# Kernel tuning notes

Hardware: AMD Instinct MI355X
Metric: run time of the kernel (lower is better)

Reference implementation:

```python
import jax, jax.numpy as jnp
import numpy as np

B, S, HID = 4, 2048, 2048
NH, NKV, D = 16, 8, 128
RK, RV = 16, 16
HPG = NH // NKV
SCALING = D ** -0.5
NEG = -1e9


def _rope(x, cos, sin):
    # x: [B, S, H, D]; cos/sin: [S, D//2]. Gemma split-half complex rotation.
    x1, x2 = jnp.split(x, 2, axis=-1)
    c = cos[None, :, None, :]
    s = sin[None, :, None, :]
    return jnp.concatenate([x1 * c - x2 * s, x1 * s + x2 * c], axis=-1)


def setup_inputs() -> dict:
    key = jax.random.key(0)
    ks = jax.random.split(key, 8)
    hidden_states = jax.random.normal(ks[0], (B, S, HID), dtype=jnp.float32)
    # RoPE frequencies (theta=10000)
    inv_freq = 1.0 / (10000.0 ** (np.arange(0, D, 2, dtype=np.float32) / D))
    ang = np.arange(S, dtype=np.float32)[:, None] * inv_freq[None, :]
    freqs_cos = jnp.asarray(np.cos(ang), dtype=jnp.float32)
    freqs_sin = jnp.asarray(np.sin(ang), dtype=jnp.float32)
    kv_write_indices = jnp.arange(S, dtype=jnp.int32)
    # causal additive mask [1,1,S,S]
    causal = jnp.tril(jnp.ones((S, S), dtype=bool))
    mask = jnp.where(causal, 0.0, NEG).astype(jnp.float32)[None, None]
    sc = 0.02
    W_q = jax.random.normal(ks[1], (NH * D, HID), dtype=jnp.float32) * sc
    W_k = jax.random.normal(ks[2], (NKV * D, HID), dtype=jnp.float32) * sc
    W_v = jax.random.normal(ks[3], (NKV * D, HID), dtype=jnp.float32) * sc
    o_proj_w = jax.random.normal(ks[4], (HID, NH * D), dtype=jnp.float32) * sc
    V_r_basis = jax.random.normal(ks[5], (NH, D, RK), dtype=jnp.float32) * (D ** -0.5)
    Z_v_basis = jax.random.normal(ks[6], (NKV, D, RV), dtype=jnp.float32) * (D ** -0.5)
    return {"hidden_states": hidden_states, "freqs_cos": freqs_cos, "freqs_sin": freqs_sin,
            "kv_write_indices": kv_write_indices, "mask": mask, "W_q": W_q, "W_k": W_k,
            "W_v": W_v, "o_proj_w": o_proj_w, "V_r_basis": V_r_basis, "Z_v_basis": Z_v_basis}


def reference(hidden_states, freqs_cos, freqs_sin, kv_write_indices, mask,
              W_q, W_k, W_v, o_proj_w, V_r_basis, Z_v_basis):
    bsz, q_len, _ = hidden_states.shape
    q = (hidden_states @ W_q.T).reshape(bsz, q_len, NH, D)
    k = (hidden_states @ W_k.T).reshape(bsz, q_len, NKV, D)
    v = (hidden_states @ W_v.T).reshape(bsz, q_len, NKV, D)

    # project K per-head onto its group's basis (vectorized over the head loop)
    head_to_group = jnp.arange(NH) // HPG                       # [NH]
    k_per_head = k[:, :, head_to_group, :]                      # [B,S,NH,D]
    pk = jnp.einsum('bshd,hdr->bshr', k_per_head, V_r_basis)    # [B,S,NH,RK]
    pv = jnp.einsum('bqgd,gdr->bqgr', v, Z_v_basis)             # [B,S,NKV,RV]

    # factorized cache write (scatter along seq dim), prefill: kv_seq_len = S
    kv_seq_len = q_len
    cache_pk = jnp.zeros((bsz, kv_seq_len, NH, RK), hidden_states.dtype)
    cache_pv = jnp.zeros((bsz, kv_seq_len, NKV, RV), hidden_states.dtype)
    cache_pk = cache_pk.at[:, kv_write_indices].set(pk)
    cache_pv = cache_pv.at[:, kv_write_indices].set(pv)

    # reconstruct K/V from compressed cache
    k_hat = jnp.einsum('bshr,hrd->bshd', cache_pk, jnp.swapaxes(V_r_basis, -1, -2))
    v_hat = jnp.einsum('bsgr,grd->bsgd', cache_pv, jnp.swapaxes(Z_v_basis, -1, -2))

    # RoPE post-reconstruction
    q_rot = _rope(q, freqs_cos[:q_len], freqs_sin[:q_len])
    k_rot = _rope(k_hat, freqs_cos[:kv_seq_len], freqs_sin[:kv_seq_len])

    # GQA: repeat kv heads
    v_g = jnp.repeat(v_hat, HPG, axis=2)                        # [B,S,NH,D]

    scores = jnp.einsum('bqhd,bkhd->bhqk', q_rot, k_rot) * SCALING
    scores = scores + mask[:, :, :q_len, :kv_seq_len]
    probs = jax.nn.softmax(scores.astype(jnp.float32), axis=-1).astype(hidden_states.dtype)
    out = jnp.einsum('bhqk,bkhd->bqhd', probs, v_g)
    out = out.reshape(bsz, q_len, NH * D)
    return out @ o_proj_w.T
```

## Files before the change

### kernel.cpp

```cpp
#include <hip/hip_runtime.h>

typedef unsigned short ushort8 __attribute__((ext_vector_type(8)));
typedef short s16x8 __attribute__((ext_vector_type(8)));
typedef float f32x4 __attribute__((ext_vector_type(4)));

#define AS1 __attribute__((address_space(1)))
#define AS3 __attribute__((address_space(3)))

#define B_    4
#define S_    2048
#define HID_  2048
#define NH_   16
#define NKV_  8
#define D_    128
#define RK_   16
#define SCALING_ 0.08838834764831845f
#define LOG2E_   1.4426950408889634f
#define NEGBIG   -1.0e30f

__device__ __forceinline__ float bf2f(unsigned short u) {
  union { unsigned int i; float f; } x; x.i = ((unsigned int)u) << 16; return x.f;
}
__device__ __forceinline__ unsigned short f2bf(float f) {
  union { float f; unsigned int i; } x; x.f = f;
  unsigned int r = x.i + 0x7fffu + ((x.i >> 16) & 1u);
  return (unsigned short)(r >> 16);
}

__global__ __launch_bounds__(256) void cvt_bf16(const float* __restrict__ in,
                                                unsigned short* __restrict__ out,
                                                int n8) {
  int i = blockIdx.x * 256 + threadIdx.x;
  const int stride = gridDim.x * 256;
  for (; i < n8; i += stride) {
    const float4 a = ((const float4*)in)[i * 2];
    const float4 b = ((const float4*)in)[i * 2 + 1];
    ushort8 u;
    u[0] = f2bf(a.x); u[1] = f2bf(a.y); u[2] = f2bf(a.z); u[3] = f2bf(a.w);
    u[4] = f2bf(b.x); u[5] = f2bf(b.y); u[6] = f2bf(b.z); u[7] = f2bf(b.w);
    *(ushort8*)&out[i * 8] = u;
  }
}

__global__ __launch_bounds__(256) void wfuse(const float* __restrict__ W_k,
                                             const float* __restrict__ W_v,
                                             const float* __restrict__ Vr,
                                             const float* __restrict__ Zv,
                                             unsigned short* __restrict__ Wf) {
  const int idx = blockIdx.x;
  const int cc = blockIdx.y * 256;
  const int tid = threadIdx.x;
  const bool isK = idx < 16;
  const int hg = isK ? idx : (idx - 16);
  const int wrow0 = isK ? (idx * 16) : (256 + (idx - 16) * 16);
  const float* W = isK ? &W_k[(size_t)((hg >> 1) * 128) * HID_]
                       : &W_v[(size_t)(hg * 128) * HID_];
  const float* P = isK ? &Vr[(size_t)hg * 128 * 16] : &Zv[(size_t)hg * 128 * 16];
  __shared__ float Wl[32][257];
  float acc[16] = {};
  for (int d0 = 0; d0 < 128; d0 += 32) {
    __syncthreads();
#pragma unroll 8
    for (int dd = 0; dd < 32; ++dd)
      Wl[dd][tid] = W[(size_t)(d0 + dd) * HID_ + cc + tid];
    __syncthreads();
#pragma unroll 8
    for (int dd = 0; dd < 32; ++dd) {
      const float w = Wl[dd][tid];
#pragma unroll
      for (int r = 0; r < 16; ++r) acc[r] += w * P[(d0 + dd) * 16 + r];
    }
  }
#pragma unroll
  for (int r = 0; r < 16; ++r)
    Wf[(size_t)(wrow0 + r) * HID_ + cc + tid] = f2bf(acc[r]);
}

template<bool CBF>
__global__ __launch_bounds__(256) void gemm_mfma(const unsigned short* __restrict__ A,
                                                 const unsigned short* __restrict__ Bb,
                                                 void* __restrict__ C_,
                                                 int M, int N, int K) {
  __shared__ unsigned short Ash[128 * 64];
  __shared__ unsigned short Bsh[128 * 64];
  const int tid = threadIdx.x;
  const int w = tid >> 6, l = tid & 63, lg = l >> 4, ll = l & 15;
  const int wr = w >> 1, wc = w & 1;
  const int flat = blockIdx.y * gridDim.x + blockIdx.x;
  const int cpx = (gridDim.x * gridDim.y) >> 3;
  const int swz = (flat & 7) * cpx + (flat >> 3);
  const int bm = (swz / gridDim.x) * 128, bn = (swz % gridDim.x) * 128;

  f32x4 acc[4][4];
#pragma unroll
  for (int i = 0; i < 4; i++)
#pragma unroll
    for (int j = 0; j < 4; j++) acc[i][j] = (f32x4){0.f, 0.f, 0.f, 0.f};

  const int srow = tid >> 3;
  const int sslot = tid & 7;

  for (int k0 = 0; k0 < K; k0 += 64) {
    __syncthreads();
#pragma unroll
    for (int c = 0; c < 4; ++c) {
      const int row = c * 32 + srow;
      const int ss = sslot ^ (row & 7);
      const unsigned short* srcA = &A[(size_t)(bm + row) * K + k0 + ss * 8];
      const unsigned short* srcB = &Bb[(size_t)(bn + row) * K + k0 + ss * 8];
      char* dstA = ((char*)Ash) + c * 4096 + w * 1024;
      char* dstB = ((char*)Bsh) + c * 4096 + w * 1024;
      __builtin_amdgcn_global_load_lds((const AS1 void*)srcA, (AS3 void*)dstA, 16, 0, 0);
      __builtin_amdgcn_global_load_lds((const AS1 void*)srcB, (AS3 void*)dstB, 16, 0, 0);
    }
    __syncthreads();

#pragma unroll
    for (int ks = 0; ks < 2; ++ks) {
      s16x8 af[4], bf_[4];
#pragma unroll
      for (int mi = 0; mi < 4; ++mi) {
        const int row = wr * 64 + mi * 16 + ll;
        af[mi] = *(const s16x8*)&Ash[row * 64 + (((ks * 4 + lg) ^ (row & 7)) * 8)];
      }
#pragma unroll
      for (int ni = 0; ni < 4; ++ni) {
        const int row = wc * 64 + ni * 16 + ll;
        bf_[ni] = *(const s16x8*)&Bsh[row * 64 + (((ks * 4 + lg) ^ (row & 7)) * 8)];
      }
#pragma unroll
      for (int mi = 0; mi < 4; ++mi)
#pragma unroll
        for (int ni = 0; ni < 4; ++ni)
          acc[mi][ni] = __builtin_amdgcn_mfma_f32_16x16x32_bf16(af[mi], bf_[ni], acc[mi][ni], 0, 0, 0);
    }
  }

#pragma unroll
  for (int mi = 0; mi < 4; ++mi)
#pragma unroll
    for (int ni = 0; ni < 4; ++ni)
#pragma unroll
      for (int j = 0; j < 4; ++j) {
        const int row = bm + wr * 64 + mi * 16 + lg * 4 + j;
        const int col = bn + wc * 64 + ni * 16 + ll;
        if (CBF) ((unsigned short*)C_)[(size_t)row * N + col] = f2bf(acc[mi][ni][j]);
        else     ((float*)C_)[(size_t)row * N + col] = acc[mi][ni][j];
      }
}

template<bool CBF>
__global__ __launch_bounds__(512) void gemm256_8ph(const unsigned short* __restrict__ A,
                                                   const unsigned short* __restrict__ Bb,
                                                   void* __restrict__ C_,
                                                   int M, int N, int K) {
  __shared__ unsigned short Lds[2][2][256 * 64];
  const int tid = threadIdx.x;
  const int w = tid >> 6, l = tid & 63, lg = l >> 4, ll = l & 15;
  const int wr = w >> 2;
  const int wc = w & 3;
  const int flat = blockIdx.y * gridDim.x + blockIdx.x;
  const int cpx = (gridDim.x * gridDim.y) >> 3;
  const int swz = (flat & 7) * cpx + (flat >> 3);
  const int bm = (swz / gridDim.x) * 256, bn = (swz % gridDim.x) * 256;

  f32x4 acc[8][4];
#pragma unroll
  for (int i = 0; i < 8; i++)
#pragma unroll
    for (int j = 0; j < 4; j++) acc[i][j] = (f32x4){0.f, 0.f, 0.f, 0.f};

  auto stage = [&](int op, int hh, int slot, int kk) {
    const unsigned short* base = (op == 0) ? A : Bb;
    const int r0 = (op == 0) ? bm : bn;
#pragma unroll
    for (int i = 0; i < 2; ++i) {
      const int r = hh * 128 + i * 64 + (tid >> 3);
      const int ss = (tid & 7) ^ (r & 7);
      const unsigned short* src = &base[(size_t)(r0 + r) * K + kk + ss * 8];
      unsigned short* dstb = &Lds[slot][op][(hh * 128 + i * 64 + (w << 3)) * 64];
      __builtin_amdgcn_global_load_lds((const AS1 void*)src, (AS3 void*)dstb, 16, 0, 0);
    }
  };

  const int NT = K >> 6;

  stage(0, 0, 0, 0);
  stage(1, 0, 0, 0);
  stage(1, 1, 0, 0);
  stage(0, 1, 0, 0);

#define GPHASE(MIH, NIH, WAITN, DO_PF)                                          \
  {                                                                             \
    if (WAITN == 4)      asm volatile("s_waitcnt vmcnt(4)" ::: "memory");       \
    else if (WAITN == 6) asm volatile("s_waitcnt vmcnt(6)" ::: "memory");       \
    __builtin_amdgcn_sched_barrier(0);                                          \
    __builtin_amdgcn_s_barrier();                                               \
    __builtin_amdgcn_sched_barrier(0);                                          \
    s16x8 af[4][2], bf_[2][2];                                                  \
    _Pragma("unroll")                                                           \
    for (int mi2 = 0; mi2 < 4; ++mi2)                                           \
      _Pragma("unroll")                                                         \
      for (int ks = 0; ks < 2; ++ks) {                                          \
        const int row = (MIH) * 128 + wr * 64 + mi2 * 16 + ll;                  \
        af[mi2][ks] = *(const s16x8*)&Lds[s][0][row * 64 +                      \
                          (((ks * 4 + lg) ^ (row & 7)) * 8)];                   \
      }                                                                         \
    _Pragma("unroll")                                                           \
    for (int ni2 = 0; ni2 < 2; ++ni2)                                           \
      _Pragma("unroll")                                                         \
      for (int ks = 0; ks < 2; ++ks) {                                          \
        const int row = (NIH) * 128 + wc * 32 + ni2 * 16 + ll;                  \
        bf_[ni2][ks] = *(const s16x8*)&Lds[s][1][row * 64 +                     \
                          (((ks * 4 + lg) ^ (row & 7)) * 8)];                   \
      }                                                                         \
    __builtin_amdgcn_s_setprio(1);                                              \
    _Pragma("unroll")                                                           \
    for (int mi2 = 0; mi2 < 4; ++mi2)                                           \
      _Pragma("unroll")                                                         \
      for (int ni2 = 0; ni2 < 2; ++ni2)                                         \
        _Pragma("unroll")                                                       \
        for (int ks = 0; ks < 2; ++ks)                                          \
          acc[(MIH) * 4 + mi2][(NIH) * 2 + ni2] =                               \
              __builtin_amdgcn_mfma_f32_16x16x32_bf16(                          \
                  af[mi2][ks], bf_[ni2][ks],                                    \
                  acc[(MIH) * 4 + mi2][(NIH) * 2 + ni2], 0, 0, 0);              \
    __builtin_amdgcn_s_setprio(0);                                              \
    DO_PF                                                                       \
  }

  for (int t = 0; t < NT; ++t) {
    const int s = t & 1;
    const int s2 = s ^ 1;
    const bool hn = (t + 1 < NT);
    const int k1 = (t + 1) << 6;
    GPHASE(0, 0, 4, { if (hn) { stage(0, 0, s2, k1); stage(1, 0, s2, k1); } })
    GPHASE(0, 1, 6, { if (hn) { stage(1, 1, s2, k1); } })
    GPHASE(1, 1, 6, { if (hn) { stage(0, 1, s2, k1); } })
    GPHASE(1, 0, 0, {})
  }
#undef GPHASE

#pragma unroll
  for (int mih = 0; mih < 2; ++mih)
#pragma unroll
    for (int mi2 = 0; mi2 < 4; ++mi2)
#pragma unroll
      for (int nih = 0; nih < 2; ++nih)
#pragma unroll
        for (int ni2 = 0; ni2 < 2; ++ni2)
#pragma unroll
          for (int j = 0; j < 4; ++j) {
            const int row = bm + mih * 128 + wr * 64 + mi2 * 16 + lg * 4 + j;
            const int col = bn + nih * 128 + wc * 32 + ni2 * 16 + ll;
            const float v = acc[mih * 4 + mi2][nih * 2 + ni2][j];
            if (CBF) ((unsigned short*)C_)[(size_t)row * N + col] = f2bf(v);
            else     ((float*)C_)[(size_t)row * N + col] = v;
          }
}

__global__ __launch_bounds__(256) void rope_q(unsigned short* __restrict__ q,
                                              const float* __restrict__ cosT,
                                              const float* __restrict__ sinT) {
  const int p = blockIdx.x * 256 + threadIdx.x;
  const int d = p & 63;
  const int h = (p >> 6) & 15;
  const int s = (p >> 10) & 2047;
  const int b = p >> 21;
  const size_t base = (((size_t)b * S_ + s) * NH_ + h) * D_ + d;
  const float x1 = bf2f(q[base]), x2 = bf2f(q[base + 64]);
  const float c = cosT[s * 64 + d], sn = sinT[s * 64 + d];
  const float sc = SCALING_ * LOG2E_;
  q[base]      = f2bf((x1 * c - x2 * sn) * sc);
  q[base + 64] = f2bf((x1 * sn + x2 * c) * sc);
}

__global__ __launch_bounds__(256) void expand_k(const float* __restrict__ pkpv,
                                                const float* __restrict__ Vr,
                                                const float* __restrict__ cosT,
                                                const float* __restrict__ sinT,
                                                unsigned short* __restrict__ kr) {
  const int s0 = blockIdx.x * 32, h = blockIdx.y, b = blockIdx.z;
  const int tid = threadIdx.x;
  __shared__ float pkS[32][17];
  if (tid < 128) {
    const int r_ = tid >> 2, c4 = (tid & 3) * 4;
    float4 v = *(const float4*)&pkpv[(size_t)(b * S_ + s0 + r_) * 384 + h * 16 + c4];
    pkS[r_][c4 + 0] = v.x; pkS[r_][c4 + 1] = v.y;
    pkS[r_][c4 + 2] = v.z; pkS[r_][c4 + 3] = v.w;
  }
  __syncthreads();
  const int row = tid >> 3, dl = tid & 7;
  float kh[16];
#pragma unroll
  for (int j = 0; j < 16; j++) {
    const int d = dl + 8 * j;
    const float4* w = (const float4*)&Vr[((size_t)h * D_ + d) * RK_];
    float a = 0.f;
#pragma unroll
    for (int q4 = 0; q4 < 4; q4++) {
      float4 wv = w[q4];
      a += pkS[row][q4 * 4 + 0] * wv.x + pkS[row][q4 * 4 + 1] * wv.y
         + pkS[row][q4 * 4 + 2] * wv.z + pkS[row][q4 * 4 + 3] * wv.w;
    }
    kh[j] = a;
  }
  const int pos = s0 + row;
  const size_t o = (((size_t)b * NH_ + h) * S_ + pos) * D_;
#pragma unroll
  for (int j = 0; j < 8; j++) {
    const int d = dl + 8 * j;
    const float c = cosT[pos * 64 + d], sn = sinT[pos * 64 + d];
    kr[o + d]      = f2bf(kh[j] * c - kh[j + 8] * sn);
    kr[o + d + 64] = f2bf(kh[j] * sn + kh[j + 8] * c);
  }
}

__global__ __launch_bounds__(256) void expand_v(const float* __restrict__ pkpv,
                                                const float* __restrict__ Zv,
                                                unsigned short* __restrict__ vh) {
  const int s0 = blockIdx.x * 32, g = blockIdx.y, b = blockIdx.z;
  const int tid = threadIdx.x;
  __shared__ float pvS[32][17];
  if (tid < 128) {
    const int r_ = tid >> 2, c4 = (tid & 3) * 4;
    float4 v = *(const float4*)&pkpv[(size_t)(b * S_ + s0 + r_) * 384 + 256 + g * 16 + c4];
    pvS[r_][c4 + 0] = v.x; pvS[r_][c4 + 1] = v.y;
    pvS[r_][c4 + 2] = v.z; pvS[r_][c4 + 3] = v.w;
  }
  __syncthreads();
  const int row = tid >> 3, dl = tid & 7;
  const size_t o = (((size_t)b * NKV_ + g) * S_ + s0 + row) * D_;
#pragma unroll
  for (int j = 0; j < 16; j++) {
    const int d = dl + 8 * j;
    const float4* w = (const float4*)&Zv[((size_t)g * D_ + d) * RK_];
    float a = 0.f;
#pragma unroll
    for (int q4 = 0; q4 < 4; q4++) {
      float4 wv = w[q4];
      a += pvS[row][q4 * 4 + 0] * wv.x + pvS[row][q4 * 4 + 1] * wv.y
         + pvS[row][q4 * 4 + 2] * wv.z + pvS[row][q4 * 4 + 3] * wv.w;
    }
    vh[o + d] = f2bf(a);
  }
}

template<bool SPLIT>
__global__ __launch_bounds__(256) void attn_mfma(const unsigned short* __restrict__ q,
                                                 const unsigned short* __restrict__ kr,
                                                 const unsigned short* __restrict__ vh,
                                                 unsigned short* __restrict__ outp,
                                                 unsigned short* __restrict__ P0,
                                                 unsigned short* __restrict__ P1,
                                                 float2* __restrict__ ml0,
                                                 float2* __restrict__ ml1) {
  int qt, h, b, half;
  if constexpr (SPLIT) {
    const int flat = ((int)blockIdx.z * 16 + (int)blockIdx.y) * 32 + (int)blockIdx.x;
    const int swz = (flat & 7) * 256 + (flat >> 3);
    qt = 15 - (swz & 15);
    half = (swz >> 4) & 1;
    h = (swz >> 5) & 15;
    b = swz >> 9;
  } else {
    const int flat = ((int)blockIdx.z * 16 + (int)blockIdx.y) * 16 + (int)blockIdx.x;
    const int swz = (flat & 7) * 128 + (flat >> 3);
    qt = 15 - (swz & 15);
    half = 0;
    h = (swz >> 4) & 15;
    b = swz >> 8;
  }
  const int g = h >> 1;
  const int tid = threadIdx.x;
  const int w = tid >> 6, l = tid & 63, lg = l >> 4, ll = l & 15;

  __shared__ unsigned short Klds[2][64 * 128];
  __shared__ unsigned short Vt[2][128 * 64];
  __shared__ unsigned short Ps[4][32 * 64];

  const int qr0 = qt * 128 + w * 32;
  const int kt0   = SPLIT ? (half ? qt + 1 : 0)          : 0;
  const int ktend = SPLIT ? (half ? 2 * qt + 1 : qt)     : 2 * qt + 1;
  const int kmy = 2 * qt + (w >> 1);

  s16x8 qf[2][4];
#pragma unroll
  for (int mi = 0; mi < 2; ++mi)
#pragma unroll
    for (int ks = 0; ks < 4; ++ks)
      qf[mi][ks] = *(const s16x8*)&q[(((size_t)b * S_ + qr0 + mi * 16 + ll) * NH_ + h) * D_ + ks * 32 + lg * 8];

  f32x4 o[2][8];
#pragma unroll
  for (int mi = 0; mi < 2; ++mi)
#pragma unroll
    for (int nd = 0; nd < 8; ++nd) o[mi][nd] = (f32x4){0.f, 0.f, 0.f, 0.f};
  float m_[2][4], l_[2][4];
#pragma unroll
  for (int mi = 0; mi < 2; ++mi)
#pragma unroll
    for (int j = 0; j < 4; ++j) { m_[mi][j] = NEGBIG; l_[mi][j] = 0.f; }

  const unsigned short* kbase = &kr[(((size_t)b * NH_ + h) * S_) * D_];
  const unsigned short* vbase = &vh[(((size_t)b * NKV_ + g) * S_) * D_];
  const int vk = (tid & 31) * 2, d0v = (tid >> 5) * 16;

  ushort8 va0, va1, vb0, vb1;
  {
    const unsigned short* kb0 = kbase + (size_t)kt0 * 64 * D_;
#pragma unroll
    for (int c = 0; c < 4; ++c) {
      const int ro = c * 16 + w * 4 + lg;
      const int ss = ll ^ (ro & 7);
      const unsigned short* src = kb0 + ro * D_ + ss * 8;
      char* dst = ((char*)&Klds[0][0]) + c * 4096 + w * 1024;
      __builtin_amdgcn_global_load_lds((const AS1 void*)src, (AS3 void*)dst, 16, 0, 0);
    }
    const unsigned short* v0 = vbase + (size_t)(kt0 * 64 + vk) * D_ + d0v;
    va0 = *(const ushort8*)v0; va1 = *(const ushort8*)(v0 + 8);
    vb0 = *(const ushort8*)(v0 + D_); vb1 = *(const ushort8*)(v0 + D_ + 8);
#pragma unroll
    for (int j = 0; j < 8; ++j) {
      const int d1 = d0v + j, d2 = d0v + 8 + j;
      *(unsigned int*)&Vt[0][d1 * 64 + (((vk >> 3) ^ (d1 & 7)) * 8) + (vk & 7)] =
          (unsigned int)va0[j] | ((unsigned int)vb0[j] << 16);
      *(unsigned int*)&Vt[0][d2 * 64 + (((vk >> 3) ^ (d2 & 7)) * 8) + (vk & 7)] =
          (unsigned int)va1[j] | ((unsigned int)vb1[j] << 16);
    }
  }
  __syncthreads();

  for (int kt = kt0; kt <= ktend; ++kt) {
    const int p = (kt - kt0) & 1;
    if (kt < ktend) {
      const unsigned short* kb2 = kbase + (size_t)(kt + 1) * 64 * D_;
#pragma unroll
      for (int c = 0; c < 4; ++c) {
        const int ro = c * 16 + w * 4 + lg;
        const int ss = ll ^ (ro & 7);
        const unsigned short* src = kb2 + ro * D_ + ss * 8;
        char* dst = ((char*)&Klds[p ^ 1][0]) + c * 4096 + w * 1024;
        __builtin_amdgcn_global_load_lds((const AS1 void*)src, (AS3 void*)dst, 16, 0, 0);
      }
      const unsigned short* v0 = vbase + (size_t)((kt + 1) * 64 + vk) * D_ + d0v;
      va0 = *(const ushort8*)v0; va1 = *(const ushort8*)(v0 + 8);
      vb0 = *(const ushort8*)(v0 + D_); vb1 = *(const ushort8*)(v0 + D_ + 8);
    }

    if (kt <= kmy) {
      f32x4 s[2][4];
#pragma unroll
      for (int mi = 0; mi < 2; ++mi)
#pragma unroll
        for (int ni = 0; ni < 4; ++ni) s[mi][ni] = (f32x4){0.f, 0.f, 0.f, 0.f};
#pragma unroll
      for (int ks = 0; ks < 4; ++ks) {
#pragma unroll
        for (int ni = 0; ni < 4; ++ni) {
          const int row = ni * 16 + ll;
          const s16x8 kf = *(const s16x8*)&Klds[p][row * 128 + (((ks * 4 + lg) ^ (row & 7)) * 8)];
          s[0][ni] = __builtin_amdgcn_mfma_f32_16x16x32_bf16(qf[0][ks], kf, s[0][ni], 0, 0, 0);
          s[1][ni] = __builtin_amdgcn_mfma_f32_16x16x32_bf16(qf[1][ks], kf, s[1][ni], 0, 0, 0);
        }
      }

      const bool diag = (kt == kmy);
      float lm[2][4];
#pragma unroll
      for (int mi = 0; mi < 2; ++mi)
#pragma unroll
        for (int j = 0; j < 4; ++j) {
          if (diag) {
            const int qg = qr0 + mi * 16 + lg * 4 + j;
#pragma unroll
            for (int ni = 0; ni < 4; ++ni)
              if (kt * 64 + ni * 16 + ll > qg) s[mi][ni][j] = NEGBIG;
          }
          lm[mi][j] = fmaxf(fmaxf(s[mi][0][j], s[mi][1][j]),
                            fmaxf(s[mi][2][j], s[mi][3][j]));
        }
      float excess = lm[0][0] - m_[0][0];
#pragma unroll
      for (int mi = 0; mi < 2; ++mi)
#pragma unroll
        for (int j = 0; j < 4; ++j) excess = fmaxf(excess, lm[mi][j] - m_[mi][j]);
      const bool slow = __any(excess > 11.5f);

#pragma unroll
      for (int mi = 0; mi < 2; ++mi)
#pragma unroll
        for (int j = 0; j < 4; ++j) {
          float ps_[4];
          if (slow) {
            float mt = lm[mi][j];
            mt = fmaxf(mt, __shfl_xor(mt, 1));
            mt = fmaxf(mt, __shfl_xor(mt, 2));
            mt = fmaxf(mt, __shfl_xor(mt, 4));
            mt = fmaxf(mt, __shfl_xor(mt, 8));
            const float mnew = fmaxf(m_[mi][j], mt);
            const float al = exp2f(m_[mi][j] - mnew);
            m_[mi][j] = mnew;
            float sum = 0.f;
#pragma unroll
            for (int ni = 0; ni < 4; ++ni) { ps_[ni] = exp2f(s[mi][ni][j] - mnew); sum += ps_[ni]; }
            l_[mi][j] = l_[mi][j] * al + sum;
#pragma unroll
            for (int nd = 0; nd < 8; ++nd) o[mi][nd][j] *= al;
          } else {
            float sum = 0.f;
#pragma unroll
            for (int ni = 0; ni < 4; ++ni) { ps_[ni] = exp2f(s[mi][ni][j] - m_[mi][j]); sum += ps_[ni]; }
            l_[mi][j] += sum;
          }
          const int prow = mi * 16 + lg * 4 + j;
#pragma unroll
          for (int nq = 0; nq < 2; ++nq) {
            unsigned int u;
            asm("v_cvt_pk_bf16_f32 %0, %1, %2" : "=v"(u) : "v"(ps_[nq * 2]), "v"(ps_[nq * 2 + 1]));
            const int c0 = nq * 32 + ll, c1 = nq * 32 + 16 + ll;
            Ps[w][prow * 64 + (((c0 >> 3) ^ (prow & 7)) * 8) + (ll & 7)] = (unsigned short)u;
            Ps[w][prow * 64 + (((c1 >> 3) ^ (prow & 7)) * 8) + (ll & 7)] = (unsigned short)(u >> 16);
          }
        }

      s16x8 pa[2][2];
#pragma unroll
      for (int mi = 0; mi < 2; ++mi)
#pragma unroll
        for (int ks2 = 0; ks2 < 2; ++ks2) {
          const int prow = mi * 16 + ll;
          pa[mi][ks2] = *(const s16x8*)&Ps[w][prow * 64 + (((ks2 * 4 + lg) ^ (prow & 7)) * 8)];
        }
#pragma unroll
      for (int nd = 0; nd < 8; ++nd) {
#pragma unroll
        for (int ks2 = 0; ks2 < 2; ++ks2) {
          const int vr = nd * 16 + ll;
          const s16x8 vbf = *(const s16x8*)&Vt[p][vr * 64 + (((ks2 * 4 + lg) ^ (vr & 7)) * 8)];
          o[0][nd] = __builtin_amdgcn_mfma_f32_16x16x32_bf16(pa[0][ks2], vbf, o[0][nd], 0, 0, 0);
          o[1][nd] = __builtin_amdgcn_mfma_f32_16x16x32_bf16(pa[1][ks2], vbf, o[1][nd], 0, 0, 0);
        }
      }
    }

    if (kt < ktend) {
#pragma unroll
      for (int j = 0; j < 8; ++j) {
        const int d1 = d0v + j, d2 = d0v + 8 + j;
        *(unsigned int*)&Vt[p ^ 1][d1 * 64 + (((vk >> 3) ^ (d1 & 7)) * 8) + (vk & 7)] =
            (unsigned int)va0[j] | ((unsigned int)vb0[j] << 16);
        *(unsigned int*)&Vt[p ^ 1][d2 * 64 + (((vk >> 3) ^ (d2 & 7)) * 8) + (vk & 7)] =
            (unsigned int)va1[j] | ((unsigned int)vb1[j] << 16);
      }
    }
    __syncthreads();
  }

#pragma unroll
  for (int mi = 0; mi < 2; ++mi)
#pragma unroll
    for (int j = 0; j < 4; ++j) {
      float ls = l_[mi][j];
      ls += __shfl_xor(ls, 1);
      ls += __shfl_xor(ls, 2);
      ls += __shfl_xor(ls, 4);
      ls += __shfl_xor(ls, 8);
      if constexpr (SPLIT) {
        unsigned short* Ph = half ? P1 : P0;
        float2* mlh = half ? ml1 : ml0;
        const size_t ridx = ((size_t)b * NH_ + h) * S_ + qr0 + mi * 16 + lg * 4 + j;
        unsigned short* op = &Ph[ridx * D_ + ll];
#pragma unroll
        for (int nd = 0; nd < 8; ++nd) op[nd * 16] = f2bf(o[mi][nd][j]);
        if (ll == 0) mlh[ridx] = make_float2(m_[mi][j], ls);
      } else {
        const float inv = 1.f / ls;
        const size_t rowg = (size_t)b * S_ + qr0 + mi * 16 + lg * 4 + j;
        unsigned short* op = &outp[rowg * (NH_ * D_) + h * D_ + ll];
#pragma unroll
        for (int nd = 0; nd < 8; ++nd) op[nd * 16] = f2bf(o[mi][nd][j] * inv);
      }
    }
}

__global__ __launch_bounds__(256) void attn_combine(const unsigned short* __restrict__ P0,
                                                    const unsigned short* __restrict__ P1,
                                                    const float2* __restrict__ ml0,
                                                    const float2* __restrict__ ml1,
                                                    unsigned short* __restrict__ outp) {
  const int s = blockIdx.x, b = blockIdx.y;
  const int tid = threadIdx.x;
  const int h = tid >> 4, d0 = (tid & 15) * 8;
  const size_t ridx = ((size_t)b * NH_ + h) * S_ + s;
  const float2 a = ml0[ridx], c = ml1[ridx];
  const float m = fmaxf(a.x, c.x);
  const float a0 = exp2f(a.x - m), a1 = exp2f(c.x - m);
  const float inv = 1.f / (a0 * a.y + a1 * c.y);
  const ushort8 u0 = *(const ushort8*)&P0[ridx * D_ + d0];
  const ushort8 u1 = *(const ushort8*)&P1[ridx * D_ + d0];
  ushort8 r;
#pragma unroll
  for (int j = 0; j < 8; ++j)
    r[j] = f2bf((a0 * bf2f(u0[j]) + a1 * bf2f(u1[j])) * inv);
  *(ushort8*)&outp[((size_t)b * S_ + s) * (NH_ * D_) + h * D_ + d0] = r;
}

extern "C" void kernel_launch(void* const* d_in, const int* in_sizes, int n_in,
                              void* d_out, int out_size, void* d_ws, size_t ws_size,
                              hipStream_t stream) {
  const float* hidden = (const float*)d_in[0];
  const float* cosT   = (const float*)d_in[1];
  const float* sinT   = (const float*)d_in[2];
  const float* W_q    = (const float*)d_in[5];
  const float* W_k    = (const float*)d_in[6];
  const float* W_v    = (const float*)d_in[7];
  const float* W_o    = (const float*)d_in[8];
  const float* Vr     = (const float*)d_in[9];
  const float* Zv     = (const float*)d_in[10];
  float* out = (float*)d_out;

  char* ws = (char*)d_ws;
  unsigned short* hb     = (unsigned short*)(ws + 0);
  unsigned short* attn_b = (unsigned short*)(ws + 0);
  unsigned short* P0     = (unsigned short*)(ws + 0);
  unsigned short* q_b    = (unsigned short*)(ws + 33554432);
  unsigned short* kr_b   = (unsigned short*)(ws + 67108864);
  unsigned short* Wf     = (unsigned short*)(ws + 100663296);
  unsigned short* vh_b   = (unsigned short*)(ws + 100663296);
  unsigned short* WR1    = (unsigned short*)(ws + 117440512);
  float*          pkpv   = (float*)(ws + 117440512);
  unsigned short* P1     = (unsigned short*)(ws + 130023424);
  float2*         ml0    = (float2*)(ws + 163577856);
  float2*         ml1    = (float2*)(ws + 164626432);
  const size_t NEED_SPLIT = 165675008ull;
  const bool split = (ws_size >= NEED_SPLIT);

  const int M = B_ * S_;

  cvt_bf16<<<2048, 256, 0, stream>>>(hidden, hb, (B_ * S_ * HID_) / 8);
  cvt_bf16<<<2048, 256, 0, stream>>>(W_q, WR1, (HID_ * HID_) / 8);
  gemm256_8ph<true><<<dim3(8, 32), 512, 0, stream>>>(hb, WR1, q_b, M, 2048, HID_);

  wfuse<<<dim3(24, 8), 256, 0, stream>>>(W_k, W_v, Vr, Zv, Wf);
  gemm_mfma<false><<<dim3(3, 64), 256, 0, stream>>>(hb, Wf, pkpv, M, 384, HID_);

  rope_q<<<(B_ * S_ * NH_ * 64) / 256, 256, 0, stream>>>(q_b, cosT, sinT);

  expand_k<<<dim3(S_ / 32, NH_, B_), 256, 0, stream>>>(pkpv, Vr, cosT, sinT, kr_b);
  expand_v<<<dim3(S_ / 32, NKV_, B_), 256, 0, stream>>>(pkpv, Zv, vh_b);

  cvt_bf16<<<2048, 256, 0, stream>>>(W_o, WR1, (HID_ * HID_) / 8);

  if (split) {
    attn_mfma<true><<<dim3(32, 16, 4), 256, 0, stream>>>(q_b, kr_b, vh_b, nullptr,
                                                         P0, P1, ml0, ml1);
    attn_combine<<<dim3(S_, B_), 256, 0, stream>>>(P0, P1, ml0, ml1, q_b);
    gemm256_8ph<false><<<dim3(8, 32), 512, 0, stream>>>(q_b, WR1, out, M, HID_, HID_);
  } else {
    attn_mfma<false><<<dim3(16, 16, 4), 256, 0, stream>>>(q_b, kr_b, vh_b, attn_b,
                                                          nullptr, nullptr, nullptr, nullptr);
    gemm256_8ph<false><<<dim3(8, 32), 512, 0, stream>>>(attn_b, WR1, out, M, HID_, HID_);
  }
}
```

Baseline: 708.0 us.

## Split attention query tile across eight waves of sixteen rows each

The attention kernel moves from 4 waves of 32 query rows to 8 waves of 16 query rows per 128-row tile, at 512 threads per block. K/V tile loads are spread over twice as many threads, and per-wave register state (Q fragments, accumulators, softmax stats) is halved. The aim is more waves to hide latency and lower register pressure. The cost is that each K/V fragment read from LDS now feeds one MFMA instead of two, which doubles LDS read traffic per FLOP, and the larger blocks add barrier cost.

```diff
diff --git a/kernel.cpp b/kernel.cpp
--- a/kernel.cpp
+++ b/kernel.cpp
@@ -347,7 +347,7 @@
 }
 
 template<bool SPLIT>
-__global__ __launch_bounds__(256) void attn_mfma(const unsigned short* __restrict__ q,
+__global__ __launch_bounds__(512) void attn_mfma(const unsigned short* __restrict__ q,
                                                  const unsigned short* __restrict__ kr,
                                                  const unsigned short* __restrict__ vh,
                                                  unsigned short* __restrict__ outp,
@@ -377,56 +377,48 @@
 
   __shared__ unsigned short Klds[2][64 * 128];
   __shared__ unsigned short Vt[2][128 * 64];
-  __shared__ unsigned short Ps[4][32 * 64];
-
-  const int qr0 = qt * 128 + w * 32;
-  const int kt0   = SPLIT ? (half ? qt + 1 : 0)          : 0;
-  const int ktend = SPLIT ? (half ? 2 * qt + 1 : qt)     : 2 * qt + 1;
-  const int kmy = 2 * qt + (w >> 1);
-
-  s16x8 qf[2][4];
-#pragma unroll
-  for (int mi = 0; mi < 2; ++mi)
-#pragma unroll
-    for (int ks = 0; ks < 4; ++ks)
-      qf[mi][ks] = *(const s16x8*)&q[(((size_t)b * S_ + qr0 + mi * 16 + ll) * NH_ + h) * D_ + ks * 32 + lg * 8];
-
-  f32x4 o[2][8];
-#pragma unroll
-  for (int mi = 0; mi < 2; ++mi)
-#pragma unroll
-    for (int nd = 0; nd < 8; ++nd) o[mi][nd] = (f32x4){0.f, 0.f, 0.f, 0.f};
-  float m_[2][4], l_[2][4];
-#pragma unroll
-  for (int mi = 0; mi < 2; ++mi)
-#pragma unroll
-    for (int j = 0; j < 4; ++j) { m_[mi][j] = NEGBIG; l_[mi][j] = 0.f; }
+  __shared__ unsigned short Ps[8][16 * 64];
+
+  const int qr0 = qt * 128 + w * 16;
+  const int kt0   = SPLIT ? (half ? qt + 1 : 0)      : 0;
+  const int ktend = SPLIT ? (half ? 2 * qt + 1 : qt) : 2 * qt + 1;
+  const int kmy = 2 * qt + (w >> 2);
+
+  s16x8 qf[4];
+#pragma unroll
+  for (int ks = 0; ks < 4; ++ks)
+    qf[ks] = *(const s16x8*)&q[(((size_t)b * S_ + qr0 + ll) * NH_ + h) * D_ + ks * 32 + lg * 8];
+
+  f32x4 o[8];
+#pragma unroll
+  for (int nd = 0; nd < 8; ++nd) o[nd] = (f32x4){0.f, 0.f, 0.f, 0.f};
+  float m_[4], l_[4];
+#pragma unroll
+  for (int j = 0; j < 4; ++j) { m_[j] = NEGBIG; l_[j] = 0.f; }
 
   const unsigned short* kbase = &kr[(((size_t)b * NH_ + h) * S_) * D_];
   const unsigned short* vbase = &vh[(((size_t)b * NKV_ + g) * S_) * D_];
-  const int vk = (tid & 31) * 2, d0v = (tid >> 5) * 16;
-
-  ushort8 va0, va1, vb0, vb1;
+  const int vk = (tid & 31) * 2;
+  const int vd0 = (tid >> 5) * 8;
+
+  ushort8 va, vb2;
   {
     const unsigned short* kb0 = kbase + (size_t)kt0 * 64 * D_;
 #pragma unroll
-    for (int c = 0; c < 4; ++c) {
-      const int ro = c * 16 + w * 4 + lg;
-      const int ss = ll ^ (ro & 7);
-      const unsigned short* src = kb0 + ro * D_ + ss * 8;
-      char* dst = ((char*)&Klds[0][0]) + c * 4096 + w * 1024;
+    for (int c = 0; c < 2; ++c) {
+      const int row = c * 32 + (tid >> 4);
+      const int ss = (tid & 15) ^ (row & 7);
+      const unsigned short* src = kb0 + row * D_ + ss * 8;
+      char* dst = ((char*)&Klds[0][0]) + c * 8192 + w * 1024;
       __builtin_amdgcn_global_load_lds((const AS1 void*)src, (AS3 void*)dst, 16, 0, 0);
     }
-    const unsigned short* v0 = vbase + (size_t)(kt0 * 64 + vk) * D_ + d0v;
-    va0 = *(const ushort8*)v0; va1 = *(const ushort8*)(v0 + 8);
-    vb0 = *(const ushort8*)(v0 + D_); vb1 = *(const ushort8*)(v0 + D_ + 8);
+    const unsigned short* v0 = vbase + (size_t)(kt0 * 64 + vk) * D_ + vd0;
+    va = *(const ushort8*)v0; vb2 = *(const ushort8*)(v0 + D_);
 #pragma unroll
     for (int j = 0; j < 8; ++j) {
-      const int d1 = d0v + j, d2 = d0v + 8 + j;
-      *(unsigned int*)&Vt[0][d1 * 64 + (((vk >> 3) ^ (d1 & 7)) * 8) + (vk & 7)] =
-          (unsigned int)va0[j] | ((unsigned int)vb0[j] << 16);
-      *(unsigned int*)&Vt[0][d2 * 64 + (((vk >> 3) ^ (d2 & 7)) * 8) + (vk & 7)] =
-          (unsigned int)va1[j] | ((unsigned int)vb1[j] << 16);
+      const int d = vd0 + j;
+      *(unsigned int*)&Vt[0][d * 64 + (((vk >> 3) ^ (d & 7)) * 8) + (vk & 7)] =
+          (unsigned int)va[j] | ((unsigned int)vb2[j] << 16);
     }
   }
   __syncthreads();
@@ -436,110 +428,94 @@
     if (kt < ktend) {
       const unsigned short* kb2 = kbase + (size_t)(kt + 1) * 64 * D_;
 #pragma unroll
-      for (int c = 0; c < 4; ++c) {
-        const int ro = c * 16 + w * 4 + lg;
-        const int ss = ll ^ (ro & 7);
-        const unsigned short* src = kb2 + ro * D_ + ss * 8;
-        char* dst = ((char*)&Klds[p ^ 1][0]) + c * 4096 + w * 1024;
+      for (int c = 0; c < 2; ++c) {
+        const int row = c * 32 + (tid >> 4);
+        const int ss = (tid & 15) ^ (row & 7);
+        const unsigned short* src = kb2 + row * D_ + ss * 8;
+        char* dst = ((char*)&Klds[p ^ 1][0]) + c * 8192 + w * 1024;
         __builtin_amdgcn_global_load_lds((const AS1 void*)src, (AS3 void*)dst, 16, 0, 0);
       }
-      const unsigned short* v0 = vbase + (size_t)((kt + 1) * 64 + vk) * D_ + d0v;
-      va0 = *(const ushort8*)v0; va1 = *(const ushort8*)(v0 + 8);
-      vb0 = *(const ushort8*)(v0 + D_); vb1 = *(const ushort8*)(v0 + D_ + 8);
+      const unsigned short* v0 = vbase + (size_t)((kt + 1) * 64 + vk) * D_ + vd0;
+      va = *(const ushort8*)v0; vb2 = *(const ushort8*)(v0 + D_);
     }
 
     if (kt <= kmy) {
-      f32x4 s[2][4];
-#pragma unroll
-      for (int mi = 0; mi < 2; ++mi)
-#pragma unroll
-        for (int ni = 0; ni < 4; ++ni) s[mi][ni] = (f32x4){0.f, 0.f, 0.f, 0.f};
+      f32x4 s[4];
+#pragma unroll
+      for (int ni = 0; ni < 4; ++ni) s[ni] = (f32x4){0.f, 0.f, 0.f, 0.f};
 #pragma unroll
       for (int ks = 0; ks < 4; ++ks) {
 #pragma unroll
         for (int ni = 0; ni < 4; ++ni) {
           const int row = ni * 16 + ll;
           const s16x8 kf = *(const s16x8*)&Klds[p][row * 128 + (((ks * 4 + lg) ^ (row & 7)) * 8)];
-          s[0][ni] = __builtin_amdgcn_mfma_f32_16x16x32_bf16(qf[0][ks], kf, s[0][ni], 0, 0, 0);
-          s[1][ni] = __builtin_amdgcn_mfma_f32_16x16x32_bf16(qf[1][ks], kf, s[1][ni], 0, 0, 0);
+          s[ni] = __builtin_amdgcn_mfma_f32_16x16x32_bf16(qf[ks], kf, s[ni], 0, 0, 0);
         }
       }
 
       const bool diag = (kt == kmy);
-      float lm[2][4];
-#pragma unroll
-      for (int mi = 0; mi < 2; ++mi)
-#pragma unroll
-        for (int j = 0; j < 4; ++j) {
-          if (diag) {
-            const int qg = qr0 + mi * 16 + lg * 4 + j;
-#pragma unroll
-            for (int ni = 0; ni < 4; ++ni)
-              if (kt * 64 + ni * 16 + ll > qg) s[mi][ni][j] = NEGBIG;
-          }
-          lm[mi][j] = fmaxf(fmaxf(s[mi][0][j], s[mi][1][j]),
-                            fmaxf(s[mi][2][j], s[mi][3][j]));
+      float lm[4];
+#pragma unroll
+      for (int j = 0; j < 4; ++j) {
+        if (diag) {
+          const int qg = qr0 + lg * 4 + j;
+#pragma unroll
+          for (int ni = 0; ni < 4; ++ni)
+            if (kt * 64 + ni * 16 + ll > qg) s[ni][j] = NEGBIG;
         }
-      float excess = lm[0][0] - m_[0][0];
-#pragma unroll
-      for (int mi = 0; mi < 2; ++mi)
-#pragma unroll
-        for (int j = 0; j < 4; ++j) excess = fmaxf(excess, lm[mi][j] - m_[mi][j]);
+        lm[j] = fmaxf(fmaxf(s[0][j], s[1][j]), fmaxf(s[2][j], s[3][j]));
+      }
+      float excess = lm[0] - m_[0];
+#pragma unroll
+      for (int j = 1; j < 4; ++j) excess = fmaxf(excess, lm[j] - m_[j]);
       const bool slow = __any(excess > 11.5f);
 
 #pragma unroll
-      for (int mi = 0; mi < 2; ++mi)
-#pragma unroll
-        for (int j = 0; j < 4; ++j) {
-          float ps_[4];
-          if (slow) {
-            float mt = lm[mi][j];
-            mt = fmaxf(mt, __shfl_xor(mt, 1));
-            mt = fmaxf(mt, __shfl_xor(mt, 2));
-            mt = fmaxf(mt, __shfl_xor(mt, 4));
-            mt = fmaxf(mt, __shfl_xor(mt, 8));
-            const float mnew = fmaxf(m_[mi][j], mt);
-            const float al = exp2f(m_[mi][j] - mnew);
-            m_[mi][j] = mnew;
-            float sum = 0.f;
-#pragma unroll
-            for (int ni = 0; ni < 4; ++ni) { ps_[ni] = exp2f(s[mi][ni][j] - mnew); sum += ps_[ni]; }
-            l_[mi][j] = l_[mi][j] * al + sum;
-#pragma unroll
-            for (int nd = 0; nd < 8; ++nd) o[mi][nd][j] *= al;
-          } else {
-            float sum = 0.f;
-#pragma unroll
-            for (int ni = 0; ni < 4; ++ni) { ps_[ni] = exp2f(s[mi][ni][j] - m_[mi][j]); sum += ps_[ni]; }
-            l_[mi][j] += sum;
-          }
-          const int prow = mi * 16 + lg * 4 + j;
-#pragma unroll
-          for (int nq = 0; nq < 2; ++nq) {
-            unsigned int u;
-            asm("v_cvt_pk_bf16_f32 %0, %1, %2" : "=v"(u) : "v"(ps_[nq * 2]), "v"(ps_[nq * 2 + 1]));
-            const int c0 = nq * 32 + ll, c1 = nq * 32 + 16 + ll;
-            Ps[w][prow * 64 + (((c0 >> 3) ^ (prow & 7)) * 8) + (ll & 7)] = (unsigned short)u;
-            Ps[w][prow * 64 + (((c1 >> 3) ^ (prow & 7)) * 8) + (ll & 7)] = (unsigned short)(u >> 16);
-          }
+      for (int j = 0; j < 4; ++j) {
+        float ps_[4];
+        if (slow) {
+          float mt = lm[j];
+          mt = fmaxf(mt, __shfl_xor(mt, 1));
+          mt = fmaxf(mt, __shfl_xor(mt, 2));
+          mt = fmaxf(mt, __shfl_xor(mt, 4));
+          mt = fmaxf(mt, __shfl_xor(mt, 8));
+          const float mnew = fmaxf(m_[j], mt);
+          const float al = exp2f(m_[j] - mnew);
+          m_[j] = mnew;
+          float sum = 0.f;
+#pragma unroll
+          for (int ni = 0; ni < 4; ++ni) { ps_[ni] = exp2f(s[ni][j] - mnew); sum += ps_[ni]; }
+          l_[j] = l_[j] * al + sum;
+#pragma unroll
+          for (int nd = 0; nd < 8; ++nd) o[nd][j] *= al;
+        } else {
+          float sum = 0.f;
+#pragma unroll
+          for (int ni = 0; ni < 4; ++ni) { ps_[ni] = exp2f(s[ni][j] - m_[j]); sum += ps_[ni]; }
+          l_[j] += sum;
         }
-
-      s16x8 pa[2][2];
-#pragma unroll
-      for (int mi = 0; mi < 2; ++mi)
-#pragma unroll
-        for (int ks2 = 0; ks2 < 2; ++ks2) {
-          const int prow = mi * 16 + ll;
-          pa[mi][ks2] = *(const s16x8*)&Ps[w][prow * 64 + (((ks2 * 4 + lg) ^ (prow & 7)) * 8)];
+        const int prow = lg * 4 + j;
+#pragma unroll
+        for (int nq = 0; nq < 2; ++nq) {
+          unsigned int u;
+          asm("v_cvt_pk_bf16_f32 %0, %1, %2" : "=v"(u) : "v"(ps_[nq * 2]), "v"(ps_[nq * 2 + 1]));
+          const int c0 = nq * 32 + ll, c1 = nq * 32 + 16 + ll;
+          Ps[w][prow * 64 + (((c0 >> 3) ^ (prow & 7)) * 8) + (ll & 7)] = (unsigned short)u;
+          Ps[w][prow * 64 + (((c1 >> 3) ^ (prow & 7)) * 8) + (ll & 7)] = (unsigned short)(u >> 16);
         }
+      }
+
+      s16x8 pa[2];
+#pragma unroll
+      for (int ks2 = 0; ks2 < 2; ++ks2)
+        pa[ks2] = *(const s16x8*)&Ps[w][ll * 64 + (((ks2 * 4 + lg) ^ (ll & 7)) * 8)];
 #pragma unroll
       for (int nd = 0; nd < 8; ++nd) {
 #pragma unroll
         for (int ks2 = 0; ks2 < 2; ++ks2) {
           const int vr = nd * 16 + ll;
           const s16x8 vbf = *(const s16x8*)&Vt[p][vr * 64 + (((ks2 * 4 + lg) ^ (vr & 7)) * 8)];
-          o[0][nd] = __builtin_amdgcn_mfma_f32_16x16x32_bf16(pa[0][ks2], vbf, o[0][nd], 0, 0, 0);
-          o[1][nd] = __builtin_amdgcn_mfma_f32_16x16x32_bf16(pa[1][ks2], vbf, o[1][nd], 0, 0, 0);
+          o[nd] = __builtin_amdgcn_mfma_f32_16x16x32_bf16(pa[ks2], vbf, o[nd], 0, 0, 0);
         }
       }
     }
@@ -547,41 +523,37 @@
     if (kt < ktend) {
 #pragma unroll
       for (int j = 0; j < 8; ++j) {
-        const int d1 = d0v + j, d2 = d0v + 8 + j;
-        *(unsigned int*)&Vt[p ^ 1][d1 * 64 + (((vk >> 3) ^ (d1 & 7)) * 8) + (vk & 7)] =
-            (unsigned int)va0[j] | ((unsigned int)vb0[j] << 16);
-        *(unsigned int*)&Vt[p ^ 1][d2 * 64 + (((vk >> 3) ^ (d2 & 7)) * 8) + (vk & 7)] =
-            (unsigned int)va1[j] | ((unsigned int)vb1[j] << 16);
+        const int d = vd0 + j;
+        *(unsigned int*)&Vt[p ^ 1][d * 64 + (((vk >> 3) ^ (d & 7)) * 8) + (vk & 7)] =
+            (unsigned int)va[j] | ((unsigned int)vb2[j] << 16);
       }
     }
     __syncthreads();
   }
 
 #pragma unroll
-  for (int mi = 0; mi < 2; ++mi)
-#pragma unroll
-    for (int j = 0; j < 4; ++j) {
-      float ls = l_[mi][j];
-      ls += __shfl_xor(ls, 1);
-      ls += __shfl_xor(ls, 2);
-      ls += __shfl_xor(ls, 4);
-      ls += __shfl_xor(ls, 8);
-      if constexpr (SPLIT) {
-        unsigned short* Ph = half ? P1 : P0;
-        float2* mlh = half ? ml1 : ml0;
-        const size_t ridx = ((size_t)b * NH_ + h) * S_ + qr0 + mi * 16 + lg * 4 + j;
-        unsigned short* op = &Ph[ridx * D_ + ll];
-#pragma unroll
-        for (int nd = 0; nd < 8; ++nd) op[nd * 16] = f2bf(o[mi][nd][j]);
-        if (ll == 0) mlh[ridx] = make_float2(m_[mi][j], ls);
-      } else {
-        const float inv = 1.f / ls;
-        const size_t rowg = (size_t)b * S_ + qr0 + mi * 16 + lg * 4 + j;
-        unsigned short* op = &outp[rowg * (NH_ * D_) + h * D_ + ll];
-#pragma unroll
-        for (int nd = 0; nd < 8; ++nd) op[nd * 16] = f2bf(o[mi][nd][j] * inv);
-      }
-    }
+  for (int j = 0; j < 4; ++j) {
+    float ls = l_[j];
+    ls += __shfl_xor(ls, 1);
+    ls += __shfl_xor(ls, 2);
+    ls += __shfl_xor(ls, 4);
+    ls += __shfl_xor(ls, 8);
+    if constexpr (SPLIT) {
+      unsigned short* Ph = half ? P1 : P0;
+      float2* mlh = half ? ml1 : ml0;
+      const size_t ridx = ((size_t)b * NH_ + h) * S_ + qr0 + lg * 4 + j;
+      unsigned short* op = &Ph[ridx * D_ + ll];
+#pragma unroll
+      for (int nd = 0; nd < 8; ++nd) op[nd * 16] = f2bf(o[nd][j]);
+      if (ll == 0) mlh[ridx] = make_float2(m_[j], ls);
+    } else {
+      const float inv = 1.f / ls;
+      const size_t rowg = (size_t)b * S_ + qr0 + lg * 4 + j;
+      unsigned short* op = &outp[rowg * (NH_ * D_) + h * D_ + ll];
+#pragma unroll
+      for (int nd = 0; nd < 8; ++nd) op[nd * 16] = f2bf(o[nd][j] * inv);
+    }
+  }
 }
 
 __global__ __launch_bounds__(256) void attn_combine(const unsigned short* __restrict__ P0,
@@ -653,12 +625,12 @@
   cvt_bf16<<<2048, 256, 0, stream>>>(W_o, WR1, (HID_ * HID_) / 8);
 
   if (split) {
-    attn_mfma<true><<<dim3(32, 16, 4), 256, 0, stream>>>(q_b, kr_b, vh_b, nullptr,
+    attn_mfma<true><<<dim3(32, 16, 4), 512, 0, stream>>>(q_b, kr_b, vh_b, nullptr,
                                                          P0, P1, ml0, ml1);
     attn_combine<<<dim3(S_, B_), 256, 0, stream>>>(P0, P1, ml0, ml1, q_b);
     gemm256_8ph<false><<<dim3(8, 32), 512, 0, stream>>>(q_b, WR1, out, M, HID_, HID_);
   } else {
-    attn_mfma<false><<<dim3(16, 16, 4), 256, 0, stream>>>(q_b, kr_b, vh_b, attn_b,
+    attn_mfma<false><<<dim3(16, 16, 4), 512, 0, stream>>>(q_b, kr_b, vh_b, attn_b,
                                                           nullptr, nullptr, nullptr, nullptr);
     gemm256_8ph<false><<<dim3(8, 32), 512, 0, stream>>>(attn_b, WR1, out, M, HID_, HID_);
   }
```

Result: slower. 1.678 ms (+137.0%).
